# Performance work log

Hardware: AMD Instinct MI355X
Metric: run time of the kernel (lower is better)

The kernel has to match this reference:

```python
import jax, jax.numpy as jnp
import numpy as np
import math

D_MODEL = 512
KEY_DIM = 128
NUM_LAYERS = 2
TEMP = 30.0
NORM_EPS = 1e-5
NORM_SCALE = math.sqrt(1.0 / (D_MODEL * 4 * 4))


def _l2norm_lastdim(x):
    # F.normalize(x, p=2, dim=-1): x / max(||x||, 1e-12)
    n = jnp.sqrt(jnp.sum(x * x, axis=-1, keepdims=True))
    return x / jnp.maximum(n, 1e-12)


def _attn(q, k, v, WK, bK):
    # q: [Sq,B,D], k: [Sk,B,D], v: [Sk,B,D] -> [Sq,B,D]
    wq = _l2norm_lastdim(q @ WK + bK)            # [Sq,B,K]
    wk = _l2norm_lastdim(k @ WK + bK)            # [Sk,B,K]
    dot = jnp.einsum('qbk,sbk->bqs', wq, wk)     # cosine sims
    aff = jax.nn.softmax(dot * TEMP, axis=-1)
    return jnp.einsum('bqs,sbd->qbd', aff, v)


def _instance_norm(x, h, w):
    # x: [HW,B,D]; InstanceL2Norm over (D,h,w) per batch element, size_average=True
    HW, B, D = x.shape
    ss = jnp.sum(x * x, axis=(0, 2))             # [B]
    factor = NORM_SCALE * jnp.sqrt((D * h * w) / (ss + NORM_EPS))
    return x * factor[None, :, None]


def _encoder(src4d, WKs, bKs):
    B, D, H, W = src4d.shape
    x = src4d.reshape(B, D, H * W).transpose(2, 0, 1)   # [HW,B,D]
    for _ in range(NUM_LAYERS):
        x = _instance_norm(x + _attn(x, x, x, WKs, bKs), H, W)
    return x  # memory [HW,B,D]


def _decoder(tgt4d, memory, pos, WKs, bKs, WKc, bKc):
    B, D, H, W = tgt4d.shape
    x = tgt4d.reshape(B, D, H * W).transpose(2, 0, 1)   # [HW,B,D]
    for _ in range(NUM_LAYERS):
        x = _instance_norm(x + _attn(x, x, x, WKs, bKs), H, W)
        mask = _attn(x, memory, pos, WKc, bKc)
        t2 = _instance_norm(x * mask, H, W)
        t3 = _attn(x, memory, memory * pos, WKc, bKc)
        t4 = _instance_norm(x + t3, H, W)
        x = _instance_norm(t2 + t4, H, W)
    feat = x.reshape(H, W, B, D).transpose(2, 3, 0, 1)  # [B,D,H,W]
    return feat


def setup_inputs() -> dict:
    key = jax.random.key(0)
    k1, k2, k3, k4, k5 = jax.random.split(key, 5)
    B, D, H, W = 16, D_MODEL, 32, 32
    std = math.sqrt(2.0 / KEY_DIM)
    return {
        'train_feat': jax.random.normal(k1, (B, D, H, W), jnp.float32),
        'test_feat': jax.random.normal(k2, (B, D, H, W), jnp.float32),
        'train_label': jax.random.uniform(k3, (B, H, W), jnp.float32),
        'WK_self': jax.random.normal(k4, (D, KEY_DIM), jnp.float32) * std,
        'bK_self': jnp.zeros((KEY_DIM,), jnp.float32),
        'WK_cross': jax.random.normal(k5, (D, KEY_DIM), jnp.float32) * std,
        'bK_cross': jnp.zeros((KEY_DIM,), jnp.float32),
    }


def reference(train_feat, test_feat, train_label, WK_self, bK_self, WK_cross, bK_cross):
    B, D, H, W = train_feat.shape
    memory = _encoder(train_feat, WK_self, bK_self)              # [HW,B,D]
    # pos: label [B,H,W] -> [HW,B,1] -> broadcast to [HW,B,D]
    pos = jnp.broadcast_to(train_label.reshape(B, H * W).T[:, :, None], (H * W, B, D))
    encoded_feat = _decoder(train_feat, memory, pos, WK_self, bK_self, WK_cross, bK_cross)
    decoded_feat = _decoder(test_feat, memory, pos, WK_self, bK_self, WK_cross, bK_cross)
    return (encoded_feat, decoded_feat)
```

## Files before the change

kernel.cpp:

```cpp
#include <hip/hip_runtime.h>
#include <math.h>

#define NB 16
#define SEQ 1024
#define DM 512
#define KD 128
#define TEMP_F 30.0f
#define NS_F 0.011048543456039805f
#define DS_F 524288.0f

#define SS_IDX(grp, b) (((grp) * 32 + (b)) * 16)
#define SS_STRIDE 1536
#define SS_STAGES 12
#define SS_FLOATS (SS_STRIDE * SS_STAGES)

#define PSTR 72

typedef short bf16x8 __attribute__((ext_vector_type(8)));
typedef float f32x4 __attribute__((ext_vector_type(4)));
typedef unsigned short us;
typedef unsigned short us4v __attribute__((ext_vector_type(4)));
typedef unsigned short us8 __attribute__((ext_vector_type(8)));

__device__ __forceinline__ us f2bf(float x) {
    union { float f; unsigned u; } v; v.f = x;
    unsigned r = v.u + 0x7fffu + ((v.u >> 16) & 1u);
    return (us)(r >> 16);
}
__device__ __forceinline__ float bf2f(us h) {
    union { unsigned u; float f; } v; v.u = ((unsigned)h) << 16;
    return v.f;
}

#define GLL16(gp, lp) __builtin_amdgcn_global_load_lds( \
    (__attribute__((address_space(1))) void*)(unsigned long long)(gp), \
    (__attribute__((address_space(3))) void*)(unsigned)(unsigned long long)(lp), 16, 0, 0)

__global__ __launch_bounds__(256) void k_transpose_in(const float* __restrict__ src,
                                                      us* __restrict__ XC,
                                                      us* __restrict__ XT) {
    __shared__ float tile[32][33];
    const int b = blockIdx.z;
    const int d0 = blockIdx.x * 32;
    const int s0 = blockIdx.y * 32;
    const int tx = threadIdx.x, ty = threadIdx.y;
    const float* p = src + (size_t)b * DM * SEQ;
    us* pt = XT + (size_t)b * DM * SEQ;
    us* pc = XC + (size_t)b * SEQ * 1024;
#pragma unroll
    for (int j = 0; j < 32; j += 8) {
        const size_t o = (size_t)(d0 + ty + j) * SEQ + s0 + tx;
        const float v = p[o];
        tile[ty + j][tx] = v;
        pt[o] = f2bf(v);
    }
    __syncthreads();
#pragma unroll
    for (int j = 0; j < 4; ++j) {
        const int s = s0 + ty + j * 8;
        const int d = d0 + tx;
        const float v = tile[tx][ty + j * 8];
        const us h = f2bf(v);
        pc[(size_t)s * 1024 + d] = h;
        pc[(size_t)s * 1024 + 512 + d] = f2bf(v - bf2f(h));
    }
}

__global__ __launch_bounds__(256) void k_mklabel(const us* __restrict__ MT,
                                                 const float* __restrict__ label,
                                                 us* __restrict__ ML) {
    const int b = blockIdx.y;
    const size_t off = ((size_t)blockIdx.x * 256 + threadIdx.x) * 8;
    const int s = (int)(off & (SEQ - 1));
    const size_t o = (size_t)b * DM * SEQ + off;
    us8 v = *(const us8*)(MT + o);
    const float4 l0 = *(const float4*)(label + (size_t)b * SEQ + s);
    const float4 l1 = *(const float4*)(label + (size_t)b * SEQ + s + 4);
    us8 r;
    r[0] = f2bf(bf2f(v[0]) * l0.x); r[1] = f2bf(bf2f(v[1]) * l0.y);
    r[2] = f2bf(bf2f(v[2]) * l0.z); r[3] = f2bf(bf2f(v[3]) * l0.w);
    r[4] = f2bf(bf2f(v[4]) * l1.x); r[5] = f2bf(bf2f(v[5]) * l1.y);
    r[6] = f2bf(bf2f(v[6]) * l1.z); r[7] = f2bf(bf2f(v[7]) * l1.w);
    *(us8*)(ML + o) = r;
}

__global__ __launch_bounds__(256) void k_wsplit(const float* __restrict__ WK,
                                                us* __restrict__ WC) {
    const int k = blockIdx.x;
    for (int d = threadIdx.x; d < DM; d += 256) {
        const float v = WK[(size_t)d * KD + k];
        const us h = f2bf(v);
        WC[(size_t)k * 1024 + d] = h;
        WC[(size_t)k * 1024 + 512 + d] = f2bf(v - bf2f(h));
    }
}

__global__ __launch_bounds__(256) void k_proj(const us* __restrict__ XC,
                                              const us* __restrict__ WC,
                                              const float* __restrict__ bK,
                                              us* __restrict__ Wout) {
    const int row0 = blockIdx.x * 32;
    __shared__ short As[32 * 64], Bs[128 * 64];
    __shared__ float ssp[2][32];
    const int tid = threadIdx.x, w = tid >> 6, l = tid & 63;
    const int wm = (w >> 1) * 16, wn = (w & 1) * 64;
    const int sr = l >> 3, sc = (((l & 7) ^ (l >> 3)) << 3);
    const int lr = l & 15, lk = (l >> 4) * 8;
    const int sx = (lr & 7) << 3;
    f32x4 acc[4] = {};
    for (int k0 = 0; k0 < 1536; k0 += 64) {
        const int ak0 = (k0 < 1024) ? k0 : k0 - 1024;
        const int bk0 = (k0 < 512) ? k0 : k0 - 512;
        GLL16(XC + (size_t)(row0 + w * 8 + sr) * 1024 + ak0 + sc, &As[w * 512]);
#pragma unroll
        for (int cc = 0; cc < 4; ++cc) {
            const int c = 4 * w + cc;
            GLL16(WC + (size_t)(c * 8 + sr) * 1024 + bk0 + sc, &Bs[c * 512]);
        }
        __syncthreads();
#pragma unroll
        for (int kc = 0; kc < 2; ++kc) {
            const int kk = kc * 32 + lk;
            const bf16x8 a = *(const bf16x8*)&As[(wm + lr) * 64 + (kk ^ sx)];
            bf16x8 bb[4];
#pragma unroll
            for (int fn = 0; fn < 4; ++fn)
                bb[fn] = *(const bf16x8*)&Bs[(wn + fn * 16 + lr) * 64 + (kk ^ sx)];
#pragma unroll
            for (int fn = 0; fn < 4; ++fn)
                acc[fn] = __builtin_amdgcn_mfma_f32_16x16x32_bf16(a, bb[fn], acc[fn], 0, 0, 0);
        }
        __syncthreads();
    }
    const int er = l & 15, eq = (l >> 4) * 4;
    const int nh = w & 1;
    float bkv[4];
#pragma unroll
    for (int fn = 0; fn < 4; ++fn) bkv[fn] = bK[wn + fn * 16 + er];
    float vv[4][4];
#pragma unroll
    for (int r = 0; r < 4; ++r) {
        float ss = 0.f;
#pragma unroll
        for (int fn = 0; fn < 4; ++fn) {
            const float t = acc[fn][r] + bkv[fn];
            vv[fn][r] = t;
            ss += t * t;
        }
#pragma unroll
        for (int o = 8; o > 0; o >>= 1) ss += __shfl_xor(ss, o, 64);
        if (er == 0) ssp[nh][wm + eq + r] = ss;
    }
    __syncthreads();
#pragma unroll
    for (int r = 0; r < 4; ++r) {
        const int rowloc = wm + eq + r;
        const float tot = ssp[0][rowloc] + ssp[1][rowloc];
        const float invn = 1.0f / fmaxf(sqrtf(tot), 1e-12f);
        const size_t ro = (size_t)(row0 + rowloc) * 256;
#pragma unroll
        for (int fn = 0; fn < 4; ++fn) {
            const float ov = vv[fn][r] * invn;
            const us h = f2bf(ov);
            Wout[ro + wn + fn * 16 + er] = h;
            Wout[ro + 128 + wn + fn * 16 + er] = f2bf(ov - bf2f(h));
        }
    }
}

__global__ __launch_bounds__(512, 2) void k_attn(const us* __restrict__ Qc,
                                                 const us* __restrict__ Kc,
                                                 const us* __restrict__ VT,
                                                 const us* __restrict__ XC,
                                                 const float* __restrict__ labelp,
                                                 float* __restrict__ MVEC,
                                                 float* __restrict__ Cout,
                                                 float* __restrict__ SS, int mode, int kvmask) {
    const int b = blockIdx.x;
    const int bkv = b & kvmask;
    const int q0 = blockIdx.y * 64;
    __shared__ short KL[2][4 * 64 * 64];
    __shared__ us PL[64 * PSTR];
    __shared__ float RSL[2][64], RLL[2][64];
    __shared__ float INVL[64], MVL[64];
    __shared__ float ps[3][8];
    const int tid = threadIdx.x, w = tid >> 6, l = tid & 63;
    const int lr = l & 15, g = l >> 4, lk = g * 8;
    const int qa = w & 3, sh = w >> 2;
    const int kx = (lr & 7) << 3;
    const us* Qb = Qc + (size_t)b * SEQ * 256;
    const us* Kb = Kc + (size_t)bkv * SEQ * 256;
    const us* Vb = VT + (size_t)bkv * DM * SEQ;
    const float* Lb = labelp ? labelp + (size_t)(bkv & 15) * SEQ : nullptr;

    const us* Qrow = Qb + (size_t)(q0 + qa * 16 + lr) * 256;
    bf16x8 qh[4], ql[4];
#pragma unroll
    for (int kc = 0; kc < 4; ++kc) {
        qh[kc] = *(const bf16x8*)(Qrow + kc * 32 + lk);
        ql[kc] = *(const bf16x8*)(Qrow + 128 + kc * 32 + lk);
    }
#pragma unroll
    for (int i = 0; i < 4; ++i) {
        const int c = w * 4 + i, p = c & 3, rg = c >> 2;
        GLL16(Kb + (size_t)(rg * 8 + (l >> 3)) * 256 + p * 64 + (((l & 7) ^ (l >> 3)) << 3),
              &KL[0][p * 4096 + rg * 512 + l * 8]);
    }
    __syncthreads();

    f32x4 acc[4][4];
#pragma unroll
    for (int m = 0; m < 4; ++m)
#pragma unroll
        for (int n = 0; n < 4; ++n) acc[m][n] = (f32x4){0.f, 0.f, 0.f, 0.f};
    float rs = 0.f, rl = 0.f;
    int cur = 0;
    for (int it = 0; it < 16; ++it) {
        const int s0 = it * 64;
        bf16x8 vb0[4];
#pragma unroll
        for (int n = 0; n < 4; ++n)
            vb0[n] = *(const bf16x8*)(Vb + (size_t)(w * 64 + n * 16 + lr) * 1024 + s0 + lk);
#pragma unroll
        for (int sn = 0; sn < 2; ++sn) {
            const int srow = sh * 32 + sn * 16 + lr;
            const int rowb = srow * 64;
            f32x4 sacc = {};
            bf16x8 kf[4];
#pragma unroll
            for (int kc = 0; kc < 4; ++kc)
                kf[kc] = *(const bf16x8*)&KL[cur][(kc >> 1) * 4096 + rowb + ((((kc & 1) << 5) + lk) ^ kx)];
            __builtin_amdgcn_s_setprio(1);
#pragma unroll
            for (int kc = 0; kc < 4; ++kc)
                sacc = __builtin_amdgcn_mfma_f32_16x16x32_bf16(kf[kc], qh[kc], sacc, 0, 0, 0);
#pragma unroll
            for (int kc = 0; kc < 4; ++kc)
                sacc = __builtin_amdgcn_mfma_f32_16x16x32_bf16(kf[kc], ql[kc], sacc, 0, 0, 0);
            __builtin_amdgcn_s_setprio(0);
#pragma unroll
            for (int kc = 0; kc < 4; ++kc)
                kf[kc] = *(const bf16x8*)&KL[cur][(2 + (kc >> 1)) * 4096 + rowb + ((((kc & 1) << 5) + lk) ^ kx)];
            __builtin_amdgcn_s_setprio(1);
#pragma unroll
            for (int kc = 0; kc < 4; ++kc)
                sacc = __builtin_amdgcn_mfma_f32_16x16x32_bf16(kf[kc], qh[kc], sacc, 0, 0, 0);
            __builtin_amdgcn_s_setprio(0);
            const int sbase = sh * 32 + sn * 16 + g * 4;
            float lb4[4] = {0.f, 0.f, 0.f, 0.f};
            if (mode == 2) {
                const float4 t = *(const float4*)(Lb + s0 + sbase);
                lb4[0] = t.x; lb4[1] = t.y; lb4[2] = t.z; lb4[3] = t.w;
            }
            us4v pw;
#pragma unroll
            for (int r = 0; r < 4; ++r) {
                const float e = __expf(fmaf(TEMP_F, sacc[r], -TEMP_F));
                rs += e;
                rl += e * lb4[r];
                pw[r] = f2bf(e);
            }
            *(us4v*)&PL[(qa * 16 + lr) * PSTR + sbase] = pw;
        }
        __syncthreads();
        bf16x8 vb1[4];
#pragma unroll
        for (int n = 0; n < 4; ++n)
            vb1[n] = *(const bf16x8*)(Vb + (size_t)(w * 64 + n * 16 + lr) * 1024 + s0 + 32 + lk);
        if (it < 15) {
            const int s1 = s0 + 64, nb2 = cur ^ 1;
#pragma unroll
            for (int i = 0; i < 4; ++i) {
                const int c = w * 4 + i, p = c & 3, rg = c >> 2;
                GLL16(Kb + (size_t)(s1 + rg * 8 + (l >> 3)) * 256 + p * 64 + (((l & 7) ^ (l >> 3)) << 3),
                      &KL[nb2][p * 4096 + rg * 512 + l * 8]);
            }
        }
        bf16x8 pa[4];
#pragma unroll
        for (int m = 0; m < 4; ++m)
            pa[m] = *(const bf16x8*)&PL[(m * 16 + lr) * PSTR + lk];
        __builtin_amdgcn_s_setprio(1);
#pragma unroll
        for (int m = 0; m < 4; ++m)
#pragma unroll
            for (int n = 0; n < 4; ++n)
                acc[m][n] = __builtin_amdgcn_mfma_f32_16x16x32_bf16(pa[m], vb0[n], acc[m][n], 0, 0, 0);
        __builtin_amdgcn_s_setprio(0);
#pragma unroll
        for (int m = 0; m < 4; ++m)
            pa[m] = *(const bf16x8*)&PL[(m * 16 + lr) * PSTR + 32 + lk];
        __builtin_amdgcn_s_setprio(1);
#pragma unroll
        for (int m = 0; m < 4; ++m)
#pragma unroll
            for (int n = 0; n < 4; ++n)
                acc[m][n] = __builtin_amdgcn_mfma_f32_16x16x32_bf16(pa[m], vb1[n], acc[m][n], 0, 0, 0);
        __builtin_amdgcn_s_setprio(0);
        __syncthreads();
        cur ^= 1;
    }

    rs += __shfl_xor(rs, 16, 64);
    rs += __shfl_xor(rs, 32, 64);
    rl += __shfl_xor(rl, 16, 64);
    rl += __shfl_xor(rl, 32, 64);
    if (g == 0) {
        RSL[sh][qa * 16 + lr] = rs;
        RLL[sh][qa * 16 + lr] = rl;
    }
    __syncthreads();
    if (tid < 64) {
        const float tot = RSL[0][tid] + RSL[1][tid];
        const float iv = 1.0f / tot;
        INVL[tid] = iv;
        const float mvv = (RLL[0][tid] + RLL[1][tid]) * iv;
        MVL[tid] = mvv;
        if (mode == 2) MVEC[(size_t)b * SEQ + q0 + tid] = mvv;
    }
    __syncthreads();

    const us* XCb = XC + (size_t)b * SEQ * 1024;
    float sa = 0.f, sb = 0.f, sab = 0.f;
#pragma unroll
    for (int m = 0; m < 4; ++m)
#pragma unroll
        for (int r = 0; r < 4; ++r) {
            const int q = m * 16 + g * 4 + r;
            const float iv = INVL[q];
            const float mvq = MVL[q];
            const int row = q0 + q;
#pragma unroll
            for (int n = 0; n < 4; ++n) {
                const int col = w * 64 + n * 16 + lr;
                float v = acc[m][n][r] * iv;
                const size_t o = ((size_t)b * SEQ + row) * DM + col;
                const size_t xo = (size_t)row * 1024 + col;
                const float x = bf2f(XCb[xo]) + bf2f(XCb[xo + 512]);
                v += x;
                sb += v * v;
                if (mode == 2) { const float a = x * mvq; sa += a * a; sab += a * v; }
                Cout[o] = v;
            }
        }
#pragma unroll
    for (int off = 32; off > 0; off >>= 1) {
        sb += __shfl_xor(sb, off, 64);
        if (mode == 2) { sa += __shfl_xor(sa, off, 64); sab += __shfl_xor(sab, off, 64); }
    }
    if (l == 0) { ps[0][w] = sb; ps[1][w] = sa; ps[2][w] = sab; }
    __syncthreads();
    if (tid == 0) {
        float t0 = 0.f, t1 = 0.f, t2 = 0.f;
#pragma unroll
        for (int i = 0; i < 8; ++i) { t0 += ps[0][i]; t1 += ps[1][i]; t2 += ps[2][i]; }
        if (mode == 1) {
            atomicAdd(&SS[SS_IDX(0, b)], t0);
        } else {
            atomicAdd(&SS[SS_IDX(0, b)], t1);
            atomicAdd(&SS[SS_IDX(1, b)], t0);
            atomicAdd(&SS[SS_IDX(2, b)], t2);
        }
    }
}

__global__ void k_zero(float* __restrict__ SSb) {
    const int i = blockIdx.x * 256 + threadIdx.x;
    if (i < SS_FLOATS) SSb[i] = 0.0f;
}

__global__ __launch_bounds__(256) void k_finish(const float* __restrict__ Tin,
                                                const us* __restrict__ XCin,
                                                const float* __restrict__ mv,
                                                const float* __restrict__ SS,
                                                us* __restrict__ XCout,
                                                us* __restrict__ XTb,
                                                float* __restrict__ XTf,
                                                int mode, int writeXC) {
    const int b = blockIdx.z;
    const int s0 = blockIdx.x * 32, d0 = blockIdx.y * 32;
    const int tx = threadIdx.x, ty = threadIdx.y;
    __shared__ float tile[32][33];
    float f1 = 0.f, f2 = 0.f, f3;
    if (mode == 0) {
        f3 = NS_F * sqrtf(DS_F / (SS[SS_IDX(0, b)] + 1e-5f));
    } else {
        const float ssa = SS[SS_IDX(0, b)], ssb = SS[SS_IDX(1, b)], ssab = SS[SS_IDX(2, b)];
        f1 = NS_F * sqrtf(DS_F / (ssa + 1e-5f));
        f2 = NS_F * sqrtf(DS_F / (ssb + 1e-5f));
        const float ssc = f1 * f1 * ssa + 2.f * f1 * f2 * ssab + f2 * f2 * ssb;
        f3 = NS_F * sqrtf(DS_F / (ssc + 1e-5f));
    }
#pragma unroll
    for (int j = 0; j < 4; ++j) {
        const int s = s0 + ty + j * 8;
        const int d = d0 + tx;
        const size_t o = ((size_t)b * SEQ + s) * DM + d;
        const size_t xo = ((size_t)b * SEQ + s) * 1024 + d;
        float v;
        if (mode == 0) v = f3 * Tin[o];
        else {
            const float x = bf2f(XCin[xo]) + bf2f(XCin[xo + 512]);
            v = f3 * (f1 * x * mv[(size_t)b * SEQ + s] + f2 * Tin[o]);
        }
        if (writeXC) {
            const us h = f2bf(v);
            XCout[xo] = h;
            XCout[xo + 512] = f2bf(v - bf2f(h));
        }
        tile[ty + j * 8][tx] = v;
    }
    __syncthreads();
#pragma unroll
    for (int j = 0; j < 4; ++j) {
        const int d = d0 + ty + j * 8;
        const int s = s0 + tx;
        const float v = tile[tx][ty + j * 8];
        const size_t o = ((size_t)b * DM + d) * SEQ + s;
        if (XTb) XTb[o] = f2bf(v);
        else if (XTf) XTf[o] = v;
    }
}

extern "C" void kernel_launch(void* const* d_in, const int* in_sizes, int n_in,
                              void* d_out, int out_size, void* d_ws, size_t ws_size,
                              hipStream_t stream) {
    const float* train_feat = (const float*)d_in[0];
    const float* test_feat  = (const float*)d_in[1];
    const float* label      = (const float*)d_in[2];
    const float* WKs        = (const float*)d_in[3];
    const float* bKs        = (const float*)d_in[4];
    const float* WKc        = (const float*)d_in[5];
    const float* bKc        = (const float*)d_in[6];
    float* out = (float*)d_out;
    float* w = (float*)d_ws;

    const size_t PB  = (size_t)SEQ * DM;
    const size_t SBD = (size_t)NB * PB;

    auto needF = [&](size_t nbat) {
        return nbat * (PB  + PB  + PB / 2  + PB / 4  + 1024 )
             + (size_t)NB * (PB / 2  + PB / 2  + PB / 4 )
             + 2 * (size_t)KD * 512  + SS_FLOATS + 4096;
    };
    const size_t wsf = ws_size / 4;
    const int nbat = (wsf >= needF(32)) ? 32 : NB;

    float* T    = w;
    us* XC      = (us*)(T + (size_t)nbat * PB);
    us* XTd     = XC + (size_t)nbat * 2 * PB;
    us* W1C     = XTd + (size_t)nbat * PB;
    us* MEMT    = W1C + (size_t)nbat * PB / 2;
    us* MEMLT   = MEMT + (size_t)NB * PB;
    us* WKMC    = MEMLT + (size_t)NB * PB;
    us* WCs     = WKMC + (size_t)NB * PB / 2;
    us* WCc     = WCs + (size_t)KD * 1024;
    float* MVEC = (float*)(WCc + (size_t)KD * 1024);
    float* SS   = MVEC + (size_t)nbat * SEQ;

    const dim3 gT_in(DM / 32, SEQ / 32, NB), bT(32, 8);

    int stage = 0;
    auto nextSS = [&]() { return SS + (size_t)(stage++) * SS_STRIDE; };

    k_zero<<<(SS_FLOATS + 255) / 256, 256, 0, stream>>>(SS);
    k_wsplit<<<KD, 256, 0, stream>>>(WKs, WCs);
    k_wsplit<<<KD, 256, 0, stream>>>(WKc, WCc);

    k_transpose_in<<<gT_in, bT, 0, stream>>>(train_feat, XC, MEMT);
    for (int l = 0; l < 2; ++l) {
        float* SSst = nextSS();
        k_proj<<<NB * SEQ / 32, 256, 0, stream>>>(XC, WCs, bKs, W1C);
        k_attn<<<dim3(NB, SEQ / 64), 512, 0, stream>>>(W1C, W1C, MEMT, XC, nullptr, nullptr, T, SSst, 1, 63);
        k_finish<<<dim3(SEQ / 32, DM / 32, NB), bT, 0, stream>>>(T, XC, nullptr, SSst, XC, MEMT, nullptr, 0, 1);
    }
    k_proj<<<NB * SEQ / 32, 256, 0, stream>>>(XC, WCc, bKc, WKMC);
    k_mklabel<<<dim3(DM * SEQ / 8 / 256, NB), 256, 0, stream>>>(MEMT, label, MEMLT);

    auto dec_layers = [&](int db, float* outp) {
        const dim3 gA(db, SEQ / 64);
        const dim3 gF(SEQ / 32, DM / 32, db);
        for (int l = 0; l < 2; ++l) {
            float* SSst = nextSS();
            k_proj<<<db * SEQ / 32, 256, 0, stream>>>(XC, WCs, bKs, W1C);
            k_attn<<<gA, 512, 0, stream>>>(W1C, W1C, XTd, XC, nullptr, nullptr, T, SSst, 1, 63);
            k_finish<<<gF, bT, 0, stream>>>(T, XC, nullptr, SSst, XC, XTd, nullptr, 0, 1);
            float* SSst2 = nextSS();
            k_proj<<<db * SEQ / 32, 256, 0, stream>>>(XC, WCc, bKc, W1C);
            k_attn<<<gA, 512, 0, stream>>>(W1C, WKMC, MEMLT, XC, label, MVEC, T, SSst2, 2, 15);
            if (l == 0)
                k_finish<<<gF, bT, 0, stream>>>(T, XC, MVEC, SSst2, XC, XTd, nullptr, 1, 1);
            else
                k_finish<<<gF, bT, 0, stream>>>(T, XC, MVEC, SSst2, XC, nullptr, outp, 1, 0);
        }
    };

    if (nbat == 32) {
        k_transpose_in<<<gT_in, bT, 0, stream>>>(train_feat, XC, XTd);
        k_transpose_in<<<gT_in, bT, 0, stream>>>(test_feat, XC + (size_t)NB * 2 * PB, XTd + (size_t)NB * PB);
        dec_layers(32, out);
    } else {
        k_transpose_in<<<gT_in, bT, 0, stream>>>(train_feat, XC, XTd);
        dec_layers(NB, out);
        k_transpose_in<<<gT_in, bT, 0, stream>>>(test_feat, XC, XTd);
        dec_layers(NB, out + SBD);
    }
}
```

Before: 959.4 us.

## Triple-buffer K tiles and double-buffer P to drop a per-iteration barrier

Result: faster. 873.6 us, median of 2 (-8.9%).

```diff
diff --git a/kernel.cpp b/kernel.cpp
--- a/kernel.cpp
+++ b/kernel.cpp
@@ -168,7 +168,7 @@
     }
 }
 
-__global__ __launch_bounds__(512, 2) void k_attn(const us* __restrict__ Qc,
+__global__ __launch_bounds__(512, 1) void k_attn(const us* __restrict__ Qc,
                                                  const us* __restrict__ Kc,
                                                  const us* __restrict__ VT,
                                                  const us* __restrict__ XC,
@@ -179,8 +179,8 @@
     const int b = blockIdx.x;
     const int bkv = b & kvmask;
     const int q0 = blockIdx.y * 64;
-    __shared__ short KL[2][4 * 64 * 64];
-    __shared__ us PL[64 * PSTR];
+    __shared__ short KL[3][4 * 64 * 64];
+    __shared__ us PL[2][64 * PSTR];
     __shared__ float RSL[2][64], RLL[2][64];
     __shared__ float INVL[64], MVL[64];
     __shared__ float ps[3][8];
@@ -201,11 +201,13 @@
         ql[kc] = *(const bf16x8*)(Qrow + 128 + kc * 32 + lk);
     }
 #pragma unroll
-    for (int i = 0; i < 4; ++i) {
-        const int c = w * 4 + i, p = c & 3, rg = c >> 2;
-        GLL16(Kb + (size_t)(rg * 8 + (l >> 3)) * 256 + p * 64 + (((l & 7) ^ (l >> 3)) << 3),
-              &KL[0][p * 4096 + rg * 512 + l * 8]);
-    }
+    for (int t = 0; t < 2; ++t)
+#pragma unroll
+        for (int i = 0; i < 4; ++i) {
+            const int c = w * 4 + i, p = c & 3, rg = c >> 2;
+            GLL16(Kb + (size_t)(t * 64 + rg * 8 + (l >> 3)) * 256 + p * 64 + (((l & 7) ^ (l >> 3)) << 3),
+                  &KL[t][p * 4096 + rg * 512 + l * 8]);
+        }
     __syncthreads();
 
     f32x4 acc[4][4];
@@ -217,10 +219,22 @@
     int cur = 0;
     for (int it = 0; it < 16; ++it) {
         const int s0 = it * 64;
+        const int pb = it & 1;
         bf16x8 vb0[4];
 #pragma unroll
         for (int n = 0; n < 4; ++n)
             vb0[n] = *(const bf16x8*)(Vb + (size_t)(w * 64 + n * 16 + lr) * 1024 + s0 + lk);
+        if (it < 14) {
+            const int stg = (cur + 2 >= 3) ? cur - 1 : cur + 2;
+            const int s2 = s0 + 128;
+#pragma unroll
+            for (int i = 0; i < 4; ++i) {
+                const int c = w * 4 + i, p = c & 3, rg = c >> 2;
+                GLL16(Kb + (size_t)(s2 + rg * 8 + (l >> 3)) * 256 + p * 64 + (((l & 7) ^ (l >> 3)) << 3),
+                      &KL[stg][p * 4096 + rg * 512 + l * 8]);
+            }
+        }
+        const short* KLc = KL[cur];
 #pragma unroll
         for (int sn = 0; sn < 2; ++sn) {
             const int srow = sh * 32 + sn * 16 + lr;
@@ -229,7 +243,7 @@
             bf16x8 kf[4];
 #pragma unroll
             for (int kc = 0; kc < 4; ++kc)
-                kf[kc] = *(const bf16x8*)&KL[cur][(kc >> 1) * 4096 + rowb + ((((kc & 1) << 5) + lk) ^ kx)];
+                kf[kc] = *(const bf16x8*)&KLc[(kc >> 1) * 4096 + rowb + ((((kc & 1) << 5) + lk) ^ kx)];
             __builtin_amdgcn_s_setprio(1);
 #pragma unroll
             for (int kc = 0; kc < 4; ++kc)
@@ -240,7 +254,7 @@
             __builtin_amdgcn_s_setprio(0);
 #pragma unroll
             for (int kc = 0; kc < 4; ++kc)
-                kf[kc] = *(const bf16x8*)&KL[cur][(2 + (kc >> 1)) * 4096 + rowb + ((((kc & 1) << 5) + lk) ^ kx)];
+                kf[kc] = *(const bf16x8*)&KLc[(2 + (kc >> 1)) * 4096 + rowb + ((((kc & 1) << 5) + lk) ^ kx)];
             __builtin_amdgcn_s_setprio(1);
 #pragma unroll
             for (int kc = 0; kc < 4; ++kc)
@@ -260,26 +274,18 @@
                 rl += e * lb4[r];
                 pw[r] = f2bf(e);
             }
-            *(us4v*)&PL[(qa * 16 + lr) * PSTR + sbase] = pw;
+            *(us4v*)&PL[pb][(qa * 16 + lr) * PSTR + sbase] = pw;
         }
         __syncthreads();
         bf16x8 vb1[4];
 #pragma unroll
         for (int n = 0; n < 4; ++n)
             vb1[n] = *(const bf16x8*)(Vb + (size_t)(w * 64 + n * 16 + lr) * 1024 + s0 + 32 + lk);
-        if (it < 15) {
-            const int s1 = s0 + 64, nb2 = cur ^ 1;
-#pragma unroll
-            for (int i = 0; i < 4; ++i) {
-                const int c = w * 4 + i, p = c & 3, rg = c >> 2;
-                GLL16(Kb + (size_t)(s1 + rg * 8 + (l >> 3)) * 256 + p * 64 + (((l & 7) ^ (l >> 3)) << 3),
-                      &KL[nb2][p * 4096 + rg * 512 + l * 8]);
-            }
-        }
+        const us* PLc = PL[pb];
         bf16x8 pa[4];
 #pragma unroll
         for (int m = 0; m < 4; ++m)
-            pa[m] = *(const bf16x8*)&PL[(m * 16 + lr) * PSTR + lk];
+            pa[m] = *(const bf16x8*)&PLc[(m * 16 + lr) * PSTR + lk];
         __builtin_amdgcn_s_setprio(1);
 #pragma unroll
         for (int m = 0; m < 4; ++m)
@@ -289,7 +295,7 @@
         __builtin_amdgcn_s_setprio(0);
 #pragma unroll
         for (int m = 0; m < 4; ++m)
-            pa[m] = *(const bf16x8*)&PL[(m * 16 + lr) * PSTR + 32 + lk];
+            pa[m] = *(const bf16x8*)&PLc[(m * 16 + lr) * PSTR + 32 + lk];
         __builtin_amdgcn_s_setprio(1);
 #pragma unroll
         for (int m = 0; m < 4; ++m)
@@ -297,14 +303,14 @@
             for (int n = 0; n < 4; ++n)
                 acc[m][n] = __builtin_amdgcn_mfma_f32_16x16x32_bf16(pa[m], vb1[n], acc[m][n], 0, 0, 0);
         __builtin_amdgcn_s_setprio(0);
-        __syncthreads();
-        cur ^= 1;
+        cur = (cur + 1 >= 3) ? 0 : cur + 1;
     }
 
     rs += __shfl_xor(rs, 16, 64);
     rs += __shfl_xor(rs, 32, 64);
     rl += __shfl_xor(rl, 16, 64);
     rl += __shfl_xor(rl, 32, 64);
+    __syncthreads();
     if (g == 0) {
         RSL[sh][qa * 16 + lr] = rs;
         RLL[sh][qa * 16 + lr] = rl;
```
